# Optimization experiments

Hardware: AMD Instinct MI355X
Metric: run time of the kernel (lower is better)

The kernel has to match this reference:

```python
import jax, jax.numpy as jnp
import numpy as np

N = 100000       # nodes
E = 1600000      # edges (avg degree 16)
IN, HID, OUT = 128, 128, 64


def setup_inputs() -> dict:
    key = jax.random.key(0)
    ks = jax.random.split(key, 8)
    x = jax.random.normal(ks[0], (N, IN), dtype=jnp.float32)
    edge_index = jax.random.randint(ks[1], (2, E), 0, N, dtype=jnp.int32)
    # Glorot-style init like PyG GCNConv
    def glorot(k, fan_in, fan_out):
        s = jnp.sqrt(6.0 / (fan_in + fan_out))
        return jax.random.uniform(k, (fan_in, fan_out), jnp.float32, -s, s)
    return {
        "x": x,
        "edge_index": edge_index,
        "W1": glorot(ks[2], IN, HID),  "b1": jnp.zeros((HID,), jnp.float32),
        "W2": glorot(ks[3], HID, HID), "b2": jnp.zeros((HID,), jnp.float32),
        "W3": glorot(ks[4], HID, OUT), "b3": jnp.zeros((OUT,), jnp.float32),
    }


def _gcn_norm(edge_index, n_nodes, dtype):
    # add self-loops, compute symmetric normalization D^-1/2 (A+I) D^-1/2
    loops = jnp.arange(n_nodes, dtype=edge_index.dtype)
    src = jnp.concatenate([edge_index[0], loops])
    dst = jnp.concatenate([edge_index[1], loops])
    deg = jax.ops.segment_sum(jnp.ones(src.shape[0], dtype), dst, num_segments=n_nodes)
    dinv = jnp.where(deg > 0, jax.lax.rsqrt(deg), 0.0)
    norm = dinv[src] * dinv[dst]  # [E+N]
    return src, dst, norm


def _gcn_conv(h, W, b, src, dst, norm, n_nodes):
    h = h @ W                                  # [N, out]
    msg = h[src] * norm[:, None]               # gather + scale per edge
    out = jax.ops.segment_sum(msg, dst, num_segments=n_nodes)  # scatter-add
    return out + b


def reference(x, edge_index, W1, b1, W2, b2, W3, b3):
    n_nodes = x.shape[0]
    src, dst, norm = _gcn_norm(edge_index, n_nodes, x.dtype)
    # layer 1 + 2: conv -> relu -> dropout(eval = identity)
    h = jax.nn.relu(_gcn_conv(x, W1, b1, src, dst, norm, n_nodes))
    h = jax.nn.relu(_gcn_conv(h, W2, b2, src, dst, norm, n_nodes))
    # final layer, no activation
    return _gcn_conv(h, W3, b3, src, dst, norm, n_nodes)
```

## Files before the change

### kernel.cpp

```cpp
#include <hip/hip_runtime.h>
#include <hip/hip_fp16.h>


typedef _Float16 half8 __attribute__((ext_vector_type(8)));
typedef float floatx4 __attribute__((ext_vector_type(4)));

struct h4 { __half2 a, b; };

constexpr int CH = 8192;

__global__ __launch_bounds__(256) void k_chist(const int* __restrict__ edst,
                                               int* __restrict__ histM, int E) {
    __shared__ int h[512];
    int tid = threadIdx.x;
    for (int i = tid; i < 512; i += 256) h[i] = 0;
    __syncthreads();
    int base = blockIdx.x * CH, end = min(E, base + CH);
    for (int e = base + tid; e < end; e += 256)
        atomicAdd(&h[edst[e] >> 8], 1);
    __syncthreads();
    int* row = histM + (size_t)blockIdx.x * 512;
    for (int i = tid; i < 512; i += 256) row[i] = h[i];
}

__global__ __launch_bounds__(512) void k_cscan(const int* __restrict__ histM,
                                               int* __restrict__ boff,
                                               int* __restrict__ gbase, int nblk) {
    __shared__ int sh[512];
    int t = threadIdx.x;
    int tot = 0;
    for (int b = 0; b < nblk; b++) tot += histM[(size_t)b * 512 + t];
    int val = tot;
    sh[t] = val;
    __syncthreads();
    for (int off = 1; off < 512; off <<= 1) {
        int o = (t >= off) ? sh[t - off] : 0;
        __syncthreads();
        val += o;
        sh[t] = val;
        __syncthreads();
    }
    int gb = val - tot;
    gbase[t] = gb;
    if (t == 511) gbase[512] = val;
    int run = gb;
    for (int b = 0; b < nblk; b++) {
        boff[(size_t)b * 512 + t] = run;
        run += histM[(size_t)b * 512 + t];
    }
}

__global__ __launch_bounds__(256) void k_cscatter(const int* __restrict__ esrc,
                                                  const int* __restrict__ edst,
                                                  const int* __restrict__ boff,
                                                  unsigned* __restrict__ stage, int E) {
    __shared__ int cur[512];
    int tid = threadIdx.x;
    const int* row = boff + (size_t)blockIdx.x * 512;
    for (int i = tid; i < 512; i += 256) cur[i] = row[i];
    __syncthreads();
    int base = blockIdx.x * CH, end = min(E, base + CH);
    for (int e = base + tid; e < end; e += 256) {
        int s = esrc[e], d = edst[e];
        int pos = atomicAdd(&cur[d >> 8], 1);
        stage[pos] = ((unsigned)(d & 255) << 24) | (unsigned)s;
    }
}

__global__ __launch_bounds__(256) void k_ffine(const unsigned* __restrict__ stage,
                                               const int* __restrict__ gbase,
                                               unsigned* __restrict__ epk,
                                               int* __restrict__ offs,
                                               float* __restrict__ dinv,
                                               int n, int Etot) {
    int b = blockIdx.x, tid = threadIdx.x;
    int seg0 = gbase[b];
    int cnt = gbase[b + 1] - seg0;
    int node0 = b << 8, nn = min(256, n - node0);
    __shared__ int hist[256], sh[256], cur[256];
    hist[tid] = 0;
    __syncthreads();
    for (int i = tid; i < cnt; i += 256)
        atomicAdd(&hist[stage[seg0 + i] >> 24], 1);
    __syncthreads();
    int v = hist[tid];
    int val = v;
    sh[tid] = val;
    __syncthreads();
    for (int off = 1; off < 256; off <<= 1) {
        int o = (tid >= off) ? sh[tid - off] : 0;
        __syncthreads();
        val += o;
        sh[tid] = val;
        __syncthreads();
    }
    int excl = val - v;
    if (tid < nn) {
        offs[node0 + tid] = seg0 + excl;
        dinv[node0 + tid] = rsqrtf((float)(v + 1));
    }
    cur[tid] = seg0 + excl;
    __syncthreads();
    for (int i = tid; i < cnt; i += 256) {
        unsigned r = stage[seg0 + i];
        int pos = atomicAdd(&cur[r >> 24], 1);
        epk[pos] = r & 0x00FFFFFFu;
    }
    if (b == 0 && tid == 0) offs[n] = Etot;
}

template <int F>
__global__ void k_wfrag(const float* __restrict__ W, _Float16* __restrict__ Wf) {
    constexpr int NT = F / 16;
    int tid = blockIdx.x * blockDim.x + threadIdx.x;
    if (tid >= 4 * NT * 64) return;
    int lane = tid & 63;
    int ct = (tid >> 6) % NT;
    int ks = tid / (64 * NT);
    int k0 = ks * 32 + (lane >> 4) * 8;
    int c  = ct * 16 + (lane & 15);
#pragma unroll
    for (int j = 0; j < 8; j++)
        Wf[(size_t)tid * 8 + j] = (_Float16)W[(k0 + j) * F + c];
}

template <int F, bool IN32>
__global__ __launch_bounds__(512) void k_gemm_mfma(const void* __restrict__ Hv,
                                                   const _Float16* __restrict__ Wf,
                                                   const float* __restrict__ dinv,
                                                   _Float16* __restrict__ T, int n) {
    constexpr int NT = F / 16;
    int wave = threadIdx.x >> 6, lane = threadIdx.x & 63;
    int row0 = blockIdx.x * 128 + wave * 16;
    int arow = min(row0 + (lane & 15), n - 1);
    int k0 = (lane >> 4) * 8;
    const _Float16* Hh = (const _Float16*)Hv;
    const float*    Hf = (const float*)Hv;
    floatx4 acc[NT];
#pragma unroll
    for (int t = 0; t < NT; t++) acc[t] = floatx4{0.f, 0.f, 0.f, 0.f};
#pragma unroll
    for (int ks = 0; ks < 4; ks++) {
        half8 a;
        if constexpr (IN32) {
            const float* p = Hf + (size_t)arow * 128 + ks * 32 + k0;
            float4 f0 = *(const float4*)p;
            float4 f1 = *(const float4*)(p + 4);
            a[0] = (_Float16)f0.x; a[1] = (_Float16)f0.y;
            a[2] = (_Float16)f0.z; a[3] = (_Float16)f0.w;
            a[4] = (_Float16)f1.x; a[5] = (_Float16)f1.y;
            a[6] = (_Float16)f1.z; a[7] = (_Float16)f1.w;
        } else {
            a = *(const half8*)(Hh + (size_t)arow * 128 + ks * 32 + k0);
        }
#pragma unroll
        for (int t = 0; t < NT; t++) {
            half8 b = *(const half8*)(Wf + ((size_t)(ks * NT + t) * 64 + lane) * 8);
            acc[t] = __builtin_amdgcn_mfma_f32_16x16x32_f16(a, b, acc[t], 0, 0, 0);
        }
    }
    int rbase = row0 + (lane >> 4) * 4;
    int cl = lane & 15;
#pragma unroll
    for (int r = 0; r < 4; r++) {
        int rr = rbase + r;
        if (rr < n) {
            float sc = dinv[rr];
#pragma unroll
            for (int t = 0; t < NT; t++)
                T[(size_t)rr * F + t * 16 + cl] = (_Float16)(acc[t][r] * sc);
        }
    }
}

template <int F, bool RELU, typename OT>
__global__ __launch_bounds__(256) void k_prop(const __half* __restrict__ T,
                                              const int* __restrict__ offs,
                                              const unsigned* __restrict__ epk,
                                              const float* __restrict__ dinv,
                                              const float* __restrict__ bias,
                                              OT* __restrict__ Out, int n) {
    constexpr int GRP = F / 4;
    int g  = (int)((blockIdx.x * blockDim.x + threadIdx.x) / GRP);
    int fl = threadIdx.x % GRP;
    if (g >= n) return;
    int j = offs[g], end = offs[g + 1];
    double a0 = 0.0, a1 = 0.0, a2 = 0.0, a3 = 0.0;
    for (; j + 4 <= end; j += 4) {
        unsigned s0 = epk[j + 0], s1 = epk[j + 1];
        unsigned s2 = epk[j + 2], s3 = epk[j + 3];
        h4 v0 = *(const h4*)&T[(size_t)s0 * F + fl * 4];
        h4 v1 = *(const h4*)&T[(size_t)s1 * F + fl * 4];
        h4 v2 = *(const h4*)&T[(size_t)s2 * F + fl * 4];
        h4 v3 = *(const h4*)&T[(size_t)s3 * F + fl * 4];
        float2 f0a = __half22float2(v0.a), f0b = __half22float2(v0.b);
        float2 f1a = __half22float2(v1.a), f1b = __half22float2(v1.b);
        float2 f2a = __half22float2(v2.a), f2b = __half22float2(v2.b);
        float2 f3a = __half22float2(v3.a), f3b = __half22float2(v3.b);
        a0 += (double)f0a.x + (double)f1a.x + (double)f2a.x + (double)f3a.x;
        a1 += (double)f0a.y + (double)f1a.y + (double)f2a.y + (double)f3a.y;
        a2 += (double)f0b.x + (double)f1b.x + (double)f2b.x + (double)f3b.x;
        a3 += (double)f0b.y + (double)f1b.y + (double)f2b.y + (double)f3b.y;
    }
    for (; j < end; j++) {
        unsigned s = epk[j];
        h4 v = *(const h4*)&T[(size_t)s * F + fl * 4];
        float2 fa = __half22float2(v.a), fb = __half22float2(v.b);
        a0 += (double)fa.x;
        a1 += (double)fa.y;
        a2 += (double)fb.x;
        a3 += (double)fb.y;
    }
    h4 vs = *(const h4*)&T[(size_t)g * F + fl * 4];
    float2 sa = __half22float2(vs.a), sb = __half22float2(vs.b);
    a0 += (double)sa.x; a1 += (double)sa.y;
    a2 += (double)sb.x; a3 += (double)sb.y;
    float dv = dinv[g];
    float4 b = *(const float4*)&bias[fl * 4];
    float r0 = (float)a0 * dv + b.x;
    float r1 = (float)a1 * dv + b.y;
    float r2 = (float)a2 * dv + b.z;
    float r3 = (float)a3 * dv + b.w;
    if (RELU) {
        r0 = fmaxf(r0, 0.f); r1 = fmaxf(r1, 0.f);
        r2 = fmaxf(r2, 0.f); r3 = fmaxf(r3, 0.f);
    }
    if constexpr (sizeof(OT) == 2) {
        h4 pk;
        pk.a = __floats2half2_rn(r0, r1);
        pk.b = __floats2half2_rn(r2, r3);
        *(h4*)&Out[(size_t)g * F + fl * 4] = pk;
    } else {
        *(float4*)&Out[(size_t)g * F + fl * 4] = float4{r0, r1, r2, r3};
    }
}

extern "C" void kernel_launch(void* const* d_in, const int* in_sizes, int n_in,
                              void* d_out, int out_size, void* d_ws, size_t ws_size,
                              hipStream_t stream) {
    const float* x  = (const float*)d_in[0];
    const int*   ei = (const int*)d_in[1];
    const float* W1 = (const float*)d_in[2];
    const float* b1 = (const float*)d_in[3];
    const float* W2 = (const float*)d_in[4];
    const float* b2 = (const float*)d_in[5];
    const float* W3 = (const float*)d_in[6];
    const float* b3 = (const float*)d_in[7];
    float* out = (float*)d_out;

    const int HID = in_sizes[3];
    const int IN  = in_sizes[2] / HID;
    const int N   = in_sizes[0] / IN;
    const int E   = in_sizes[1] / 2;
    const int NBC  = (N + 255) >> 8;
    const int NBLK = (E + CH - 1) / CH;

    const int* esrc = ei;
    const int* edst = ei + E;

    char* p = (char*)d_ws;
    auto alloc = [&](size_t bytes) {
        void* r = (void*)p;
        p += (bytes + 255) & ~(size_t)255;
        return r;
    };
    float*    dinv  = (float*)alloc((size_t)N * 4);
    int*      offs  = (int*)alloc((size_t)(N + 1) * 4);
    int*      histM = (int*)alloc((size_t)NBLK * 512 * 4);
    int*      boff  = (int*)alloc((size_t)NBLK * 512 * 4);
    int*      gbase = (int*)alloc((size_t)513 * 4);
    unsigned* stage = (unsigned*)alloc((size_t)E * 4);
    unsigned* epk   = (unsigned*)alloc((size_t)E * 4);
    _Float16* t0    = (_Float16*)alloc((size_t)N * 128 * 2);
    _Float16* h0    = (_Float16*)alloc((size_t)N * 128 * 2);
    _Float16* wf1   = (_Float16*)alloc((size_t)128 * 128 * 2);
    _Float16* wf2   = (_Float16*)alloc((size_t)128 * 128 * 2);
    _Float16* wf3   = (_Float16*)alloc((size_t)128 * 64 * 2);
    (void)ws_size; (void)n_in; (void)out_size;

    const int B = 256;
    k_chist<<<NBLK, B, 0, stream>>>(edst, histM, E);
    k_cscan<<<1, 512, 0, stream>>>(histM, boff, gbase, NBLK);
    k_cscatter<<<NBLK, B, 0, stream>>>(esrc, edst, boff, stage, E);
    k_ffine<<<NBC, B, 0, stream>>>(stage, gbase, epk, offs, dinv, N, E);
    k_wfrag<128><<<8, B, 0, stream>>>(W1, wf1);
    k_wfrag<128><<<8, B, 0, stream>>>(W2, wf2);
    k_wfrag<64><<<4, B, 0, stream>>>(W3, wf3);

    const int gb    = (N + 127) / 128;
    const int pb128 = (int)(((size_t)N * 32 + B - 1) / B);
    const int pb64  = (int)(((size_t)N * 16 + B - 1) / B);
    k_gemm_mfma<128, true><<<gb, 512, 0, stream>>>(x, wf1, dinv, t0, N);
    k_prop<128, true, __half><<<pb128, B, 0, stream>>>((const __half*)t0, offs, epk, dinv, b1, (__half*)h0, N);
    k_gemm_mfma<128, false><<<gb, 512, 0, stream>>>(h0, wf2, dinv, t0, N);
    k_prop<128, true, __half><<<pb128, B, 0, stream>>>((const __half*)t0, offs, epk, dinv, b2, (__half*)h0, N);
    k_gemm_mfma<64, false><<<gb, 512, 0, stream>>>(h0, wf3, dinv, t0, N);
    k_prop<64, false, float><<<pb64, B, 0, stream>>>((const __half*)t0, offs, epk, dinv, b3, out, N);
}
```

Before: 409.6 us.

## Use float accumulators in propagation, merge weight-fragment kernels, halve histogram chunk

The gather-sum propagation kernel now accumulates in fp32 instead of fp64, which removes double-precision adds and conversions from the hot edge loop. The three weight-fragment conversion launches are merged into one kernel with 20 blocks to cut launch overhead. The edge-histogram chunk size is halved, giving more blocks (and more histogram rows to scan) in the CSR build. The fp32 accumulation slightly changes rounding relative to the double version.

New measurement: 444.8 us. 1.09x slower.

```diff
diff --git a/kernel.cpp b/kernel.cpp
--- a/kernel.cpp
+++ b/kernel.cpp
@@ -7,7 +7,7 @@
 
 struct h4 { __half2 a, b; };
 
-constexpr int CH = 8192;
+constexpr int CH = 4096;
 
 __global__ __launch_bounds__(256) void k_chist(const int* __restrict__ edst,
                                                int* __restrict__ histM, int E) {
@@ -109,10 +109,18 @@
     if (b == 0 && tid == 0) offs[n] = Etot;
 }
 
-template <int F>
-__global__ void k_wfrag(const float* __restrict__ W, _Float16* __restrict__ Wf) {
-    constexpr int NT = F / 16;
-    int tid = blockIdx.x * blockDim.x + threadIdx.x;
+__global__ void k_wfrag3(const float* __restrict__ W1, _Float16* __restrict__ Wf1,
+                         const float* __restrict__ W2, _Float16* __restrict__ Wf2,
+                         const float* __restrict__ W3, _Float16* __restrict__ Wf3) {
+    int blk = blockIdx.x;
+    const float* W;
+    _Float16* Wf;
+    int F;
+    if (blk < 8)      { W = W1; Wf = Wf1; F = 128; blk -= 0; }
+    else if (blk < 16){ W = W2; Wf = Wf2; F = 128; blk -= 8; }
+    else              { W = W3; Wf = Wf3; F = 64;  blk -= 16; }
+    int NT = F / 16;
+    int tid = blk * 256 + threadIdx.x;
     if (tid >= 4 * NT * 64) return;
     int lane = tid & 63;
     int ct = (tid >> 6) % NT;
@@ -185,7 +193,7 @@
     int fl = threadIdx.x % GRP;
     if (g >= n) return;
     int j = offs[g], end = offs[g + 1];
-    double a0 = 0.0, a1 = 0.0, a2 = 0.0, a3 = 0.0;
+    float a0 = 0.f, a1 = 0.f, a2 = 0.f, a3 = 0.f;
     for (; j + 4 <= end; j += 4) {
         unsigned s0 = epk[j + 0], s1 = epk[j + 1];
         unsigned s2 = epk[j + 2], s3 = epk[j + 3];
@@ -197,30 +205,30 @@
         float2 f1a = __half22float2(v1.a), f1b = __half22float2(v1.b);
         float2 f2a = __half22float2(v2.a), f2b = __half22float2(v2.b);
         float2 f3a = __half22float2(v3.a), f3b = __half22float2(v3.b);
-        a0 += (double)f0a.x + (double)f1a.x + (double)f2a.x + (double)f3a.x;
-        a1 += (double)f0a.y + (double)f1a.y + (double)f2a.y + (double)f3a.y;
-        a2 += (double)f0b.x + (double)f1b.x + (double)f2b.x + (double)f3b.x;
-        a3 += (double)f0b.y + (double)f1b.y + (double)f2b.y + (double)f3b.y;
+        a0 += f0a.x + f1a.x + f2a.x + f3a.x;
+        a1 += f0a.y + f1a.y + f2a.y + f3a.y;
+        a2 += f0b.x + f1b.x + f2b.x + f3b.x;
+        a3 += f0b.y + f1b.y + f2b.y + f3b.y;
     }
     for (; j < end; j++) {
         unsigned s = epk[j];
         h4 v = *(const h4*)&T[(size_t)s * F + fl * 4];
         float2 fa = __half22float2(v.a), fb = __half22float2(v.b);
-        a0 += (double)fa.x;
-        a1 += (double)fa.y;
-        a2 += (double)fb.x;
-        a3 += (double)fb.y;
+        a0 += fa.x;
+        a1 += fa.y;
+        a2 += fb.x;
+        a3 += fb.y;
     }
     h4 vs = *(const h4*)&T[(size_t)g * F + fl * 4];
     float2 sa = __half22float2(vs.a), sb = __half22float2(vs.b);
-    a0 += (double)sa.x; a1 += (double)sa.y;
-    a2 += (double)sb.x; a3 += (double)sb.y;
+    a0 += sa.x; a1 += sa.y;
+    a2 += sb.x; a3 += sb.y;
     float dv = dinv[g];
     float4 b = *(const float4*)&bias[fl * 4];
-    float r0 = (float)a0 * dv + b.x;
-    float r1 = (float)a1 * dv + b.y;
-    float r2 = (float)a2 * dv + b.z;
-    float r3 = (float)a3 * dv + b.w;
+    float r0 = a0 * dv + b.x;
+    float r1 = a1 * dv + b.y;
+    float r2 = a2 * dv + b.z;
+    float r3 = a3 * dv + b.w;
     if (RELU) {
         r0 = fmaxf(r0, 0.f); r1 = fmaxf(r1, 0.f);
         r2 = fmaxf(r2, 0.f); r3 = fmaxf(r3, 0.f);
@@ -283,9 +291,7 @@
     k_cscan<<<1, 512, 0, stream>>>(histM, boff, gbase, NBLK);
     k_cscatter<<<NBLK, B, 0, stream>>>(esrc, edst, boff, stage, E);
     k_ffine<<<NBC, B, 0, stream>>>(stage, gbase, epk, offs, dinv, N, E);
-    k_wfrag<128><<<8, B, 0, stream>>>(W1, wf1);
-    k_wfrag<128><<<8, B, 0, stream>>>(W2, wf2);
-    k_wfrag<64><<<4, B, 0, stream>>>(W3, wf3);
+    k_wfrag3<<<20, B, 0, stream>>>(W1, wf1, W2, wf2, W3, wf3);
 
     const int gb    = (N + 127) / 128;
     const int pb128 = (int)(((size_t)N * 32 + B - 1) / B);
```
